# Optimization experiments

Measured on AMD Instinct MI355X. Metric: run time of the kernel, lower is better.

The kernel has to match this reference:

```python
import jax, jax.numpy as jnp
import numpy as np

N = 200000      # nodes
E = 200000      # edges per direction
IN = 256        # in_dim
HID = 256       # hidden_dim
HEADS = 4
C = HID // HEADS  # 64 per-head channels
OUT = 128
EPS = 1e-5      # LayerNorm eps (torch default)


def _ln(x, g, b):
    m = jnp.mean(x, axis=-1, keepdims=True)
    v = jnp.mean(jnp.square(x - m), axis=-1, keepdims=True)
    return (x - m) / jnp.sqrt(v + EPS) * g + b


def _gat(x, W, att_src, att_dst, bias, edge_index):
    """PyG GATConv (default args: add_self_loops=True, negative_slope=0.2, concat heads)."""
    n = x.shape[0]
    loops = jnp.arange(n, dtype=edge_index.dtype)
    ei = jnp.concatenate([edge_index, jnp.stack([loops, loops])], axis=1)
    src, dst = ei[0], ei[1]
    h = (x @ W).reshape(n, HEADS, C)                      # [N,H,C]
    a_src = jnp.sum(h * att_src, axis=-1)                 # [N,H]
    a_dst = jnp.sum(h * att_dst, axis=-1)                 # [N,H]
    e = jax.nn.leaky_relu(a_src[src] + a_dst[dst], 0.2)   # [E+N,H]
    m = jax.ops.segment_max(e, dst, num_segments=n)       # per-dst softmax max
    ex = jnp.exp(e - m[dst])
    denom = jax.ops.segment_sum(ex, dst, num_segments=n)
    alpha = ex / denom[dst]                               # [E+N,H]
    out = jax.ops.segment_sum(h[src] * alpha[..., None], dst, num_segments=n)
    return out.reshape(n, HEADS * C) + bias


def setup_inputs() -> dict:
    key = jax.random.key(0)
    ks = jax.random.split(key, 20)
    w = lambda k, s, sc=0.05: jax.random.normal(k, s, jnp.float32) * sc
    return {
        "x": jax.random.normal(ks[0], (N, IN), jnp.float32),
        "edge_index_bu": jax.random.randint(ks[1], (2, E), 0, N, jnp.int32),
        "edge_index_td": jax.random.randint(ks[2], (2, E), 0, N, jnp.int32),
        "Wp": w(ks[3], (IN, HID)), "bp": jnp.zeros((HID,), jnp.float32),
        "W_bu": w(ks[4], (HID, HID)), "asrc_bu": w(ks[5], (HEADS, C)),
        "adst_bu": w(ks[6], (HEADS, C)), "bias_bu": jnp.zeros((HID,), jnp.float32),
        "W_td": w(ks[7], (HID, HID)), "asrc_td": w(ks[8], (HEADS, C)),
        "adst_td": w(ks[9], (HEADS, C)), "bias_td": jnp.zeros((HID,), jnp.float32),
        "Wf": w(ks[10], (2 * HID, OUT)), "bf": jnp.zeros((OUT,), jnp.float32),
        "g_bu": jnp.ones((HID,), jnp.float32), "b_bu": jnp.zeros((HID,), jnp.float32),
        "g_td": jnp.ones((HID,), jnp.float32), "b_td": jnp.zeros((HID,), jnp.float32),
        "g_out": jnp.ones((OUT,), jnp.float32), "b_out": jnp.zeros((OUT,), jnp.float32),
    }


def reference(x, edge_index_bu, edge_index_td, Wp, bp,
              W_bu, asrc_bu, adst_bu, bias_bu,
              W_td, asrc_td, adst_td, bias_td,
              Wf, bf, g_bu, b_bu, g_td, b_td, g_out, b_out):
    h = jax.nn.relu(x @ Wp + bp)  # dropout is identity in eval
    x_bu = jax.nn.relu(_ln(_gat(h, W_bu, asrc_bu, adst_bu, bias_bu, edge_index_bu), g_bu, b_bu))
    x_td = jax.nn.relu(_ln(_gat(h, W_td, asrc_td, adst_td, bias_td, edge_index_td), g_td, b_td))
    out = jnp.concatenate([x_bu, x_td], axis=-1) @ Wf + bf
    out = _ln(out, g_out, b_out)
    nrm = jnp.sqrt(jnp.sum(jnp.square(out), axis=-1, keepdims=True))
    return out / jnp.maximum(nrm, 1e-12)
```

## Files before the change

### kernel.cpp

```cpp
#include <hip/hip_runtime.h>
#include <hip/hip_bf16.h>
#include <stdint.h>


typedef __attribute__((ext_vector_type(8))) short bf16x8;
typedef __attribute__((ext_vector_type(4))) short bf16x4;
typedef __attribute__((ext_vector_type(4))) float f32x4;

#define HID 256
#define HEADS 4
#define CH 64

__device__ __forceinline__ float wred(float v) {
    #pragma unroll
    for (int o = 32; o > 0; o >>= 1) v += __shfl_xor(v, o, 64);
    return v;
}
__device__ __forceinline__ float red16(float v) {
    #pragma unroll
    for (int o = 1; o < 16; o <<= 1) v += __shfl_xor(v, o, 64);
    return v;
}
__device__ __forceinline__ float bf2f(short s) {
    return __uint_as_float(((unsigned)(unsigned short)s) << 16);
}
__device__ __forceinline__ float sel4(float a0, float a1, float a2, float a3, int h) {
    return h == 0 ? a0 : (h == 1 ? a1 : (h == 2 ? a2 : a3));
}

__device__ __forceinline__ void gload_lds16(const void* g, void* l) {
    __builtin_amdgcn_global_load_lds(
        reinterpret_cast<const __attribute__((address_space(1))) uint32_t*>(
            reinterpret_cast<uintptr_t>(g)),
        reinterpret_cast<__attribute__((address_space(3))) uint32_t*>(
            reinterpret_cast<uintptr_t>(l)),
        16, 0, 0);
}

__global__ __launch_bounds__(256) void cvt_bf16(const float* __restrict__ src,
                                                __hip_bfloat16* __restrict__ dst, long n8) {
    long i = (long)blockIdx.x * 256 + threadIdx.x;
    if (i >= n8) return;
    f32x4 v0 = *(const f32x4*)(src + i * 8);
    f32x4 v1 = *(const f32x4*)(src + i * 8 + 4);
    __hip_bfloat16 o[8];
    o[0] = __float2bfloat16(v0[0]); o[1] = __float2bfloat16(v0[1]);
    o[2] = __float2bfloat16(v0[2]); o[3] = __float2bfloat16(v0[3]);
    o[4] = __float2bfloat16(v1[0]); o[5] = __float2bfloat16(v1[1]);
    o[6] = __float2bfloat16(v1[2]); o[7] = __float2bfloat16(v1[3]);
    *(bf16x8*)((short*)dst + i * 8) = *(const bf16x8*)o;
}

__global__ void transpose_w(const float* __restrict__ W,
                            __hip_bfloat16* __restrict__ Wt, int KI, int KO) {
    int idx = blockIdx.x * 256 + threadIdx.x;
    if (idx >= KI * KO) return;
    int k = idx / KO, j = idx % KO;
    Wt[(long)j * KI + k] = __float2bfloat16(W[idx]);
}

template<int BN, int MODE>
__global__ __launch_bounds__(512) void gemm_tiled(
    const __hip_bfloat16* __restrict__ A0, const __hip_bfloat16* __restrict__ A1,
    int lda, int kSplit,
    const __hip_bfloat16* __restrict__ Bt, int KI,
    const float* __restrict__ bias, int doRelu,
    __hip_bfloat16* __restrict__ outB, float* __restrict__ outF,
    const float* __restrict__ asrcW, const float* __restrict__ adstW,
    float* __restrict__ aS, float* __restrict__ aD,
    const float* __restrict__ gw, const float* __restrict__ bw, int N) {

    constexpr int WN = BN / 64;
    constexpr int WM = 8 / WN;
    constexpr int MR = (128 / WM) / 16;

    __shared__ __align__(16) __hip_bfloat16 sA[128 * 32];
    __shared__ __align__(16) __hip_bfloat16 sB[BN * 32];
    __shared__ float sRed[MODE == 2 ? 128 * 4 : 4];
    __shared__ float sN2[MODE == 2 ? 128 * 2 : 2];

    int tid = threadIdx.x;
    int wv = tid >> 6, ln = tid & 63;
    int m = ln & 15, q = ln >> 4;
    long row0 = (long)blockIdx.x * 128;
    int wr = (wv / WN) * (128 / WM);
    int wc = (wv % WN) * 64;

    f32x4 acc[MR][4];
    #pragma unroll
    for (int mi = 0; mi < MR; ++mi)
        #pragma unroll
        for (int t = 0; t < 4; ++t) acc[mi][t] = (f32x4){0.f, 0.f, 0.f, 0.f};

    int oA = tid * 16;
    long rowA = row0 + (oA >> 6);
    if (rowA >= N) rowA = N - 1;
    long aOff = rowA * lda + ((oA & 63) >> 1);

    for (int k0 = 0; k0 < KI; k0 += 32) {
        const __hip_bfloat16* Ab = (k0 < kSplit) ? A0 + k0 : A1 + (k0 - kSplit);
        __syncthreads();
        gload_lds16(Ab + aOff, (char*)sA + oA);
        #pragma unroll
        for (int j = 0; j < BN / 128; ++j) {
            int o = j * 8192 + tid * 16;
            const __hip_bfloat16* src = Bt + (long)(o >> 6) * KI + k0 + ((o & 63) >> 1);
            gload_lds16(src, (char*)sB + o);
        }
        __syncthreads();

        bf16x8 af[MR], bfr[4];
        #pragma unroll
        for (int mi = 0; mi < MR; ++mi)
            af[mi] = *(const bf16x8*)((const char*)sA + ((wr + mi * 16 + m) << 6) + q * 16);
        #pragma unroll
        for (int t = 0; t < 4; ++t)
            bfr[t] = *(const bf16x8*)((const char*)sB + ((wc + t * 16 + m) << 6) + q * 16);
        #pragma unroll
        for (int mi = 0; mi < MR; ++mi)
            #pragma unroll
            for (int t = 0; t < 4; ++t)
                acc[mi][t] = __builtin_amdgcn_mfma_f32_16x16x32_bf16(af[mi], bfr[t],
                                                                     acc[mi][t], 0, 0, 0);
    }

    if constexpr (MODE != 2) {
        #pragma unroll
        for (int mi = 0; mi < MR; ++mi) {
            #pragma unroll
            for (int t = 0; t < 4; ++t) {
                int col = wc + t * 16 + m;
                float bv = bias ? bias[col] : 0.f;
                #pragma unroll
                for (int r = 0; r < 4; ++r) {
                    long row = row0 + wr + mi * 16 + q * 4 + r;
                    if (row < N) {
                        float v = acc[mi][t][r] + bv;
                        if (doRelu) v = fmaxf(v, 0.f);
                        outB[row * BN + col] = __float2bfloat16(v);
                    }
                }
            }
        }
    }

    if constexpr (MODE == 1) {
        int h = wc >> 6;
        f32x4 sw, dw;
        #pragma unroll
        for (int t = 0; t < 4; ++t) {
            sw[t] = asrcW[wc + t * 16 + m];
            dw[t] = adstW[wc + t * 16 + m];
        }
        #pragma unroll
        for (int mi = 0; mi < MR; ++mi) {
            #pragma unroll
            for (int r = 0; r < 4; ++r) {
                float ps = acc[mi][0][r] * sw[0] + acc[mi][1][r] * sw[1]
                         + acc[mi][2][r] * sw[2] + acc[mi][3][r] * sw[3];
                float pd = acc[mi][0][r] * dw[0] + acc[mi][1][r] * dw[1]
                         + acc[mi][2][r] * dw[2] + acc[mi][3][r] * dw[3];
                ps = red16(ps); pd = red16(pd);
                long row = row0 + wr + mi * 16 + q * 4 + r;
                if (m == 0 && row < N) {
                    aS[row * 4 + h] = ps;
                    aD[row * 4 + h] = pd;
                }
            }
        }
    }

    if constexpr (MODE == 2) {
        float vv[MR][4][4];
        float gcol[4], bcol[4];
        #pragma unroll
        for (int t = 0; t < 4; ++t) {
            int col = wc + t * 16 + m;
            float bb = bias[col];
            gcol[t] = gw[col]; bcol[t] = bw[col];
            #pragma unroll
            for (int mi = 0; mi < MR; ++mi)
                #pragma unroll
                for (int r = 0; r < 4; ++r) vv[mi][t][r] = acc[mi][t][r] + bb;
        }
        int wcid = wc >> 6;
        #pragma unroll
        for (int mi = 0; mi < MR; ++mi) {
            #pragma unroll
            for (int r = 0; r < 4; ++r) {
                float s1 = vv[mi][0][r] + vv[mi][1][r] + vv[mi][2][r] + vv[mi][3][r];
                float s2 = vv[mi][0][r] * vv[mi][0][r] + vv[mi][1][r] * vv[mi][1][r]
                         + vv[mi][2][r] * vv[mi][2][r] + vv[mi][3][r] * vv[mi][3][r];
                s1 = red16(s1); s2 = red16(s2);
                if (m == 0) {
                    int lrow = wr + mi * 16 + q * 4 + r;
                    sRed[lrow * 4 + wcid * 2 + 0] = s1;
                    sRed[lrow * 4 + wcid * 2 + 1] = s2;
                }
            }
        }
        __syncthreads();
        #pragma unroll
        for (int mi = 0; mi < MR; ++mi) {
            #pragma unroll
            for (int r = 0; r < 4; ++r) {
                int lrow = wr + mi * 16 + q * 4 + r;
                float S1 = sRed[lrow * 4 + 0] + sRed[lrow * 4 + 2];
                float S2 = sRed[lrow * 4 + 1] + sRed[lrow * 4 + 3];
                float mean = S1 * (1.f / 128.f);
                float var = S2 * (1.f / 128.f) - mean * mean;
                float inv = rsqrtf(fmaxf(var, 0.f) + 1e-5f);
                float n2 = 0.f;
                #pragma unroll
                for (int t = 0; t < 4; ++t) {
                    float y = (vv[mi][t][r] - mean) * inv * gcol[t] + bcol[t];
                    vv[mi][t][r] = y;
                    n2 += y * y;
                }
                n2 = red16(n2);
                if (m == 0) sN2[lrow * 2 + wcid] = n2;
            }
        }
        __syncthreads();
        #pragma unroll
        for (int mi = 0; mi < MR; ++mi) {
            #pragma unroll
            for (int r = 0; r < 4; ++r) {
                int lrow = wr + mi * 16 + q * 4 + r;
                long row = row0 + lrow;
                float nrm = sqrtf(sN2[lrow * 2] + sN2[lrow * 2 + 1]);
                float sc = 1.f / fmaxf(nrm, 1e-12f);
                if (row < N) {
                    #pragma unroll
                    for (int t = 0; t < 4; ++t)
                        outF[row * 128 + wc + t * 16 + m] = vv[mi][t][r] * sc;
                }
            }
        }
    }
}

__global__ __launch_bounds__(256) void hist_dst(const int* __restrict__ ei, int E,
                                                int* __restrict__ cnt) {
    int e = blockIdx.x * 256 + threadIdx.x;
    if (e < E) atomicAdd(&cnt[ei[E + e]], 1);
}

__global__ __launch_bounds__(256) void scan1(const int* __restrict__ cnt,
                                             int* __restrict__ offpart,
                                             int* __restrict__ bsum, int n) {
    int t = threadIdx.x, i = blockIdx.x * 256 + t;
    int lane = t & 63, w = t >> 6;
    int v = (i < n) ? cnt[i] : 0;
    int inc = v;
    #pragma unroll
    for (int o = 1; o < 64; o <<= 1) {
        int u = __shfl_up(inc, o, 64);
        if (lane >= o) inc += u;
    }
    __shared__ int wsum[4];
    if (lane == 63) wsum[w] = inc;
    __syncthreads();
    int wadd = 0;
    #pragma unroll
    for (int k = 0; k < 4; ++k) if (k < w) wadd += wsum[k];
    if (i < n) offpart[i] = inc - v + wadd;
    if (t == 255) bsum[blockIdx.x] = inc + wadd;
}

__global__ __launch_bounds__(256) void scan2(const int* __restrict__ bsum,
                                             int* __restrict__ btot, int nb) {
    int t = threadIdx.x, lane = t & 63, w = t >> 6;
    int loc[4]; int s = 0;
    #pragma unroll
    for (int k = 0; k < 4; ++k) {
        int idx = t * 4 + k;
        int v = (idx < nb) ? bsum[idx] : 0;
        loc[k] = s; s += v;
    }
    int inc = s;
    #pragma unroll
    for (int o = 1; o < 64; o <<= 1) {
        int u = __shfl_up(inc, o, 64);
        if (lane >= o) inc += u;
    }
    __shared__ int wsum[4];
    if (lane == 63) wsum[w] = inc;
    __syncthreads();
    int wadd = 0;
    #pragma unroll
    for (int k = 0; k < 4; ++k) if (k < w) wadd += wsum[k];
    int excl = inc - s + wadd;
    #pragma unroll
    for (int k = 0; k < 4; ++k) {
        int idx = t * 4 + k;
        if (idx < nb) btot[idx] = excl + loc[k];
    }
}

__global__ __launch_bounds__(256) void finalize_off(const int* __restrict__ offpart,
                                                    const int* __restrict__ btot,
                                                    int* __restrict__ off, int n, int E) {
    int i = blockIdx.x * 256 + threadIdx.x;
    if (i < n) off[i] = offpart[i] + btot[i >> 8];
    if (i == 0) off[n] = E;
}

__global__ __launch_bounds__(256) void scatter_src(const int* __restrict__ ei, int E,
                                                   const int* __restrict__ off,
                                                   int* __restrict__ cur,
                                                   int* __restrict__ esrc) {
    int e = blockIdx.x * 256 + threadIdx.x;
    if (e >= E) return;
    int d = ei[E + e];
    int pos = off[d] + atomicAdd(&cur[d], 1);
    esrc[pos] = ei[e];
}

__global__ __launch_bounds__(256) void gat_gather(
    const int* __restrict__ off, const int* __restrict__ esrc,
    const float* __restrict__ a_s, const float* __restrict__ a_d,
    const __hip_bfloat16* __restrict__ hw,
    const float* __restrict__ bias, const float* __restrict__ g,
    const float* __restrict__ b,
    __hip_bfloat16* __restrict__ out, int N) {
    int lane = threadIdx.x & 63;
    long d = (long)blockIdx.x * 4 + (threadIdx.x >> 6);
    if (d >= N) return;
    int beg = off[d], end = off[d + 1];
    f32x4 adv = *(const f32x4*)(a_d + 4 * d);
    f32x4 asd = *(const f32x4*)(a_s + 4 * d);
    int hh = lane & 3;
    float adh_l = sel4(adv[0], adv[1], adv[2], adv[3], hh);
    float ash_l = sel4(asd[0], asd[1], asd[2], asd[3], hh);
    float es_l = ash_l + adh_l; es_l = es_l > 0.f ? es_l : 0.2f * es_l;
    float m_l = es_l, sum_l = 1.f;
    if (lane < 4) {
        for (int j = beg; j < end; ++j) {
            int s = esrc[j];
            float e = a_s[4 * (long)s + lane] + adh_l;
            e = e > 0.f ? e : 0.2f * e;
            m_l = fmaxf(m_l, e);
        }
        sum_l = __expf(es_l - m_l);
        for (int j = beg; j < end; ++j) {
            int s = esrc[j];
            float e = a_s[4 * (long)s + lane] + adh_l;
            e = e > 0.f ? e : 0.2f * e;
            sum_l += __expf(e - m_l);
        }
    }
    int h4 = lane >> 4;
    float mh = __shfl(m_l, h4, 64);
    float rsh = 1.f / __shfl(sum_l, h4, 64);
    float adh = sel4(adv[0], adv[1], adv[2], adv[3], h4);
    float esh = sel4(asd[0], asd[1], asd[2], asd[3], h4) + adh;
    esh = esh > 0.f ? esh : 0.2f * esh;
    int c0 = lane * 4;
    float acc0, acc1, acc2, acc3;
    {
        float alpha = __expf(esh - mh) * rsh;
        bf16x4 hv = *(const bf16x4*)(hw + d * HID + c0);
        acc0 = alpha * bf2f(hv[0]); acc1 = alpha * bf2f(hv[1]);
        acc2 = alpha * bf2f(hv[2]); acc3 = alpha * bf2f(hv[3]);
    }
    for (int j = beg; j < end; ++j) {
        int s = esrc[j];
        float as_h = a_s[4 * (long)s + h4];
        float e = as_h + adh; e = e > 0.f ? e : 0.2f * e;
        float alpha = __expf(e - mh) * rsh;
        bf16x4 hv = *(const bf16x4*)(hw + (long)s * HID + c0);
        acc0 += alpha * bf2f(hv[0]); acc1 += alpha * bf2f(hv[1]);
        acc2 += alpha * bf2f(hv[2]); acc3 += alpha * bf2f(hv[3]);
    }
    f32x4 bi = *(const f32x4*)(bias + c0);
    acc0 += bi[0]; acc1 += bi[1]; acc2 += bi[2]; acc3 += bi[3];
    float mean = wred(acc0 + acc1 + acc2 + acc3) * (1.f / 256.f);
    acc0 -= mean; acc1 -= mean; acc2 -= mean; acc3 -= mean;
    float var = wred(acc0 * acc0 + acc1 * acc1 + acc2 * acc2 + acc3 * acc3) * (1.f / 256.f);
    float inv = rsqrtf(var + 1e-5f);
    f32x4 gv = *(const f32x4*)(g + c0);
    f32x4 bv = *(const f32x4*)(b + c0);
    __hip_bfloat16 t0 = __float2bfloat16(fmaxf(acc0 * inv * gv[0] + bv[0], 0.f));
    __hip_bfloat16 t1 = __float2bfloat16(fmaxf(acc1 * inv * gv[1] + bv[1], 0.f));
    __hip_bfloat16 t2 = __float2bfloat16(fmaxf(acc2 * inv * gv[2] + bv[2], 0.f));
    __hip_bfloat16 t3 = __float2bfloat16(fmaxf(acc3 * inv * gv[3] + bv[3], 0.f));
    __hip_bfloat16* orow = out + d * HID + c0;
    orow[0] = t0; orow[1] = t1; orow[2] = t2; orow[3] = t3;
}

extern "C" void kernel_launch(void* const* d_in, const int* in_sizes, int n_in,
                              void* d_out, int out_size, void* d_ws, size_t ws_size,
                              hipStream_t stream) {
    const float* x      = (const float*)d_in[0];
    const int*   ei_bu  = (const int*)d_in[1];
    const int*   ei_td  = (const int*)d_in[2];
    const float* Wp     = (const float*)d_in[3];
    const float* bp     = (const float*)d_in[4];
    const float* W_bu   = (const float*)d_in[5];
    const float* asrc_bu= (const float*)d_in[6];
    const float* adst_bu= (const float*)d_in[7];
    const float* bias_bu= (const float*)d_in[8];
    const float* W_td   = (const float*)d_in[9];
    const float* asrc_td= (const float*)d_in[10];
    const float* adst_td= (const float*)d_in[11];
    const float* bias_td= (const float*)d_in[12];
    const float* Wf     = (const float*)d_in[13];
    const float* bfv    = (const float*)d_in[14];
    const float* g_bu   = (const float*)d_in[15];
    const float* b_bu   = (const float*)d_in[16];
    const float* g_td   = (const float*)d_in[17];
    const float* b_td   = (const float*)d_in[18];
    const float* g_out  = (const float*)d_in[19];
    const float* b_out  = (const float*)d_in[20];

    const int N = in_sizes[0] / HID;
    const int E = in_sizes[1] / 2;

    char* ws = (char*)d_ws;
    size_t off0 = 0;
    auto take = [&](size_t bytes) -> char* {
        char* p = ws + off0;
        off0 += (bytes + 255) & ~(size_t)255;
        return p;
    };
    __hip_bfloat16* xbf   = (__hip_bfloat16*)take((size_t)N * HID * 2);
    __hip_bfloat16* h_buf = (__hip_bfloat16*)take((size_t)N * HID * 2);
    __hip_bfloat16* xbu   = (__hip_bfloat16*)take((size_t)N * HID * 2);
    __hip_bfloat16* xtd   = (__hip_bfloat16*)take((size_t)N * HID * 2);
    float* a_s   = (float*)take((size_t)N * 16);
    float* a_d   = (float*)take((size_t)N * 16);
    int* cnt     = (int*)take((size_t)N * 4);
    int* cur     = (int*)take((size_t)N * 4);
    int* offpart = (int*)take((size_t)N * 4);
    int* offarr  = (int*)take((size_t)(N + 1) * 4);
    int* esrc    = (int*)take((size_t)E * 4);
    int* bsum    = (int*)take(1024 * 4);
    int* btot    = (int*)take(1024 * 4);
    __hip_bfloat16* Wpt  = (__hip_bfloat16*)take(256 * 256 * 2);
    __hip_bfloat16* Wbut = (__hip_bfloat16*)take(256 * 256 * 2);
    __hip_bfloat16* Wtdt = (__hip_bfloat16*)take(256 * 256 * 2);
    __hip_bfloat16* Wft  = (__hip_bfloat16*)take(512 * 128 * 2);
    __hip_bfloat16* hw = xbf;

    transpose_w<<<(256 * 256 + 255) / 256, 256, 0, stream>>>(Wp, Wpt, 256, 256);
    transpose_w<<<(256 * 256 + 255) / 256, 256, 0, stream>>>(W_bu, Wbut, 256, 256);
    transpose_w<<<(256 * 256 + 255) / 256, 256, 0, stream>>>(W_td, Wtdt, 256, 256);
    transpose_w<<<(512 * 128 + 255) / 256, 256, 0, stream>>>(Wf, Wft, 512, 128);
    long nx8 = (long)N * HID / 8;
    cvt_bf16<<<(nx8 + 255) / 256, 256, 0, stream>>>(x, xbf, nx8);

    int gm = (N + 127) / 128;

    gemm_tiled<256, 0><<<gm, 512, 0, stream>>>(xbf, xbf, HID, HID, Wpt, HID,
                                               bp, 1, h_buf, nullptr,
                                               nullptr, nullptr, nullptr, nullptr,
                                               nullptr, nullptr, N);

    const int* eis[2] = {ei_bu, ei_td};
    const __hip_bfloat16* Wts[2] = {Wbut, Wtdt};
    const float* asrcs[2] = {asrc_bu, asrc_td};
    const float* adsts[2] = {adst_bu, adst_td};
    const float* biases[2]= {bias_bu, bias_td};
    const float* gs[2]    = {g_bu, g_td};
    const float* bs[2]    = {b_bu, b_td};
    __hip_bfloat16* xouts[2] = {xbu, xtd};

    int egrid = (E + 255) / 256;
    int ngrid = (N + 255) / 256;
    int nb = (N + 255) / 256;
    for (int dir = 0; dir < 2; ++dir) {
        gemm_tiled<256, 1><<<gm, 512, 0, stream>>>(h_buf, h_buf, HID, HID, Wts[dir], HID,
                                                   nullptr, 0, hw, nullptr,
                                                   asrcs[dir], adsts[dir], a_s, a_d,
                                                   nullptr, nullptr, N);
        hipMemsetAsync(cnt, 0, (size_t)N * 8, stream);
        hist_dst<<<egrid, 256, 0, stream>>>(eis[dir], E, cnt);
        scan1<<<nb, 256, 0, stream>>>(cnt, offpart, bsum, N);
        scan2<<<1, 256, 0, stream>>>(bsum, btot, nb);
        finalize_off<<<ngrid, 256, 0, stream>>>(offpart, btot, offarr, N, E);
        scatter_src<<<egrid, 256, 0, stream>>>(eis[dir], E, offarr, cur, esrc);
        gat_gather<<<(N + 3) / 4, 256, 0, stream>>>(offarr, esrc, a_s, a_d, hw,
                                                    biases[dir], gs[dir], bs[dir],
                                                    xouts[dir], N);
    }

    gemm_tiled<128, 2><<<gm, 512, 0, stream>>>(xbu, xtd, HID, HID, Wft, 512,
                                               bfv, 0, nullptr, (float*)d_out,
                                               nullptr, nullptr, nullptr, nullptr,
                                               g_out, b_out, N);
}
```

Measured before the change: 996.8 us.

## Fuse fp32-to-bf16 conversion into GEMM, merge direction GEMMs, precompute attention alphas

Converts x from fp32 to bf16 inside the first GEMM's A-tile load, which removes the separate conversion pass and its bf16 copy. The two GAT projection GEMMs become one 512-wide GEMM with concatenated weights, and it writes attention logits for both directions. A new per-node kernel precomputes the softmax alphas per edge, so the gather kernel only streams features, now with 16 lanes per node and 16 channels each. Outputs go into one concatenated buffer that the final GEMM reads directly. The cost is an extra alpha buffer, a kernel that reads each edge's logits three times, and a one-pass variance formula that is less numerically robust.

```diff
diff --git a/kernel.cpp b/kernel.cpp
--- a/kernel.cpp
+++ b/kernel.cpp
@@ -8,14 +8,7 @@
 typedef __attribute__((ext_vector_type(4))) float f32x4;
 
 #define HID 256
-#define HEADS 4
-#define CH 64
-
-__device__ __forceinline__ float wred(float v) {
-    #pragma unroll
-    for (int o = 32; o > 0; o >>= 1) v += __shfl_xor(v, o, 64);
-    return v;
-}
+
 __device__ __forceinline__ float red16(float v) {
     #pragma unroll
     for (int o = 1; o < 16; o <<= 1) v += __shfl_xor(v, o, 64);
@@ -23,9 +16,6 @@
 }
 __device__ __forceinline__ float bf2f(short s) {
     return __uint_as_float(((unsigned)(unsigned short)s) << 16);
-}
-__device__ __forceinline__ float sel4(float a0, float a1, float a2, float a3, int h) {
-    return h == 0 ? a0 : (h == 1 ? a1 : (h == 2 ? a2 : a3));
 }
 
 __device__ __forceinline__ void gload_lds16(const void* g, void* l) {
@@ -37,20 +27,6 @@
         16, 0, 0);
 }
 
-__global__ __launch_bounds__(256) void cvt_bf16(const float* __restrict__ src,
-                                                __hip_bfloat16* __restrict__ dst, long n8) {
-    long i = (long)blockIdx.x * 256 + threadIdx.x;
-    if (i >= n8) return;
-    f32x4 v0 = *(const f32x4*)(src + i * 8);
-    f32x4 v1 = *(const f32x4*)(src + i * 8 + 4);
-    __hip_bfloat16 o[8];
-    o[0] = __float2bfloat16(v0[0]); o[1] = __float2bfloat16(v0[1]);
-    o[2] = __float2bfloat16(v0[2]); o[3] = __float2bfloat16(v0[3]);
-    o[4] = __float2bfloat16(v1[0]); o[5] = __float2bfloat16(v1[1]);
-    o[6] = __float2bfloat16(v1[2]); o[7] = __float2bfloat16(v1[3]);
-    *(bf16x8*)((short*)dst + i * 8) = *(const bf16x8*)o;
-}
-
 __global__ void transpose_w(const float* __restrict__ W,
                             __hip_bfloat16* __restrict__ Wt, int KI, int KO) {
     int idx = blockIdx.x * 256 + threadIdx.x;
@@ -59,15 +35,16 @@
     Wt[(long)j * KI + k] = __float2bfloat16(W[idx]);
 }
 
-template<int BN, int MODE>
+template<int BN, int MODE, int CVT>
 __global__ __launch_bounds__(512) void gemm_tiled(
-    const __hip_bfloat16* __restrict__ A0, const __hip_bfloat16* __restrict__ A1,
-    int lda, int kSplit,
+    const float* __restrict__ Af, const __hip_bfloat16* __restrict__ Ab, int lda,
     const __hip_bfloat16* __restrict__ Bt, int KI,
     const float* __restrict__ bias, int doRelu,
     __hip_bfloat16* __restrict__ outB, float* __restrict__ outF,
-    const float* __restrict__ asrcW, const float* __restrict__ adstW,
-    float* __restrict__ aS, float* __restrict__ aD,
+    const float* __restrict__ asrc0, const float* __restrict__ adst0,
+    const float* __restrict__ asrc1, const float* __restrict__ adst1,
+    float* __restrict__ aS0, float* __restrict__ aD0,
+    float* __restrict__ aS1, float* __restrict__ aD1,
     const float* __restrict__ gw, const float* __restrict__ bw, int N) {
 
     constexpr int WN = BN / 64;
@@ -95,12 +72,27 @@
     int oA = tid * 16;
     long rowA = row0 + (oA >> 6);
     if (rowA >= N) rowA = N - 1;
-    long aOff = rowA * lda + ((oA & 63) >> 1);
+    int kel = (oA & 63) >> 1;
+    long aBase = rowA * (long)lda + kel;
 
     for (int k0 = 0; k0 < KI; k0 += 32) {
-        const __hip_bfloat16* Ab = (k0 < kSplit) ? A0 + k0 : A1 + (k0 - kSplit);
+        f32x4 fa0, fa1;
+        if constexpr (CVT) {
+            const float* src = Af + aBase + k0;
+            fa0 = *(const f32x4*)src;
+            fa1 = *(const f32x4*)(src + 4);
+        }
         __syncthreads();
-        gload_lds16(Ab + aOff, (char*)sA + oA);
+        if constexpr (CVT) {
+            __hip_bfloat16 t8[8];
+            t8[0] = __float2bfloat16(fa0[0]); t8[1] = __float2bfloat16(fa0[1]);
+            t8[2] = __float2bfloat16(fa0[2]); t8[3] = __float2bfloat16(fa0[3]);
+            t8[4] = __float2bfloat16(fa1[0]); t8[5] = __float2bfloat16(fa1[1]);
+            t8[6] = __float2bfloat16(fa1[2]); t8[7] = __float2bfloat16(fa1[3]);
+            *(bf16x8*)((char*)sA + oA) = *(const bf16x8*)t8;
+        } else {
+            gload_lds16(Ab + aBase + k0, (char*)sA + oA);
+        }
         #pragma unroll
         for (int j = 0; j < BN / 128; ++j) {
             int o = j * 8192 + tid * 16;
@@ -145,12 +137,18 @@
     }
 
     if constexpr (MODE == 1) {
-        int h = wc >> 6;
+        int dir = wc >> 8;
+        int cc = wc & 255;
+        int h = cc >> 6;
+        const float* as_ = dir ? asrc1 : asrc0;
+        const float* ad_ = dir ? adst1 : adst0;
+        float* aS = dir ? aS1 : aS0;
+        float* aD = dir ? aD1 : aD0;
         f32x4 sw, dw;
         #pragma unroll
         for (int t = 0; t < 4; ++t) {
-            sw[t] = asrcW[wc + t * 16 + m];
-            dw[t] = adstW[wc + t * 16 + m];
+            sw[t] = as_[cc + t * 16 + m];
+            dw[t] = ad_[cc + t * 16 + m];
         }
         #pragma unroll
         for (int mi = 0; mi < MR; ++mi) {
@@ -317,76 +315,134 @@
     esrc[pos] = ei[e];
 }
 
+__global__ __launch_bounds__(256) void att_alpha(
+    const int* __restrict__ off, const int* __restrict__ esrc,
+    const float* __restrict__ a_s, const float* __restrict__ a_d,
+    float* __restrict__ alpha_self, float* __restrict__ alpha_e, int N) {
+    int d = blockIdx.x * 256 + threadIdx.x;
+    if (d >= N) return;
+    int beg = off[d], end = off[d + 1];
+    f32x4 adv = *(const f32x4*)(a_d + 4 * (long)d);
+    f32x4 asd = *(const f32x4*)(a_s + 4 * (long)d);
+    float es[4], m[4];
+    #pragma unroll
+    for (int h = 0; h < 4; ++h) {
+        float e = asd[h] + adv[h]; e = e > 0.f ? e : 0.2f * e;
+        es[h] = e; m[h] = e;
+    }
+    for (int j = beg; j < end; ++j) {
+        int s = esrc[j];
+        f32x4 asv = *(const f32x4*)(a_s + 4 * (long)s);
+        #pragma unroll
+        for (int h = 0; h < 4; ++h) {
+            float e = asv[h] + adv[h]; e = e > 0.f ? e : 0.2f * e;
+            m[h] = fmaxf(m[h], e);
+        }
+    }
+    float sum[4];
+    #pragma unroll
+    for (int h = 0; h < 4; ++h) sum[h] = __expf(es[h] - m[h]);
+    for (int j = beg; j < end; ++j) {
+        int s = esrc[j];
+        f32x4 asv = *(const f32x4*)(a_s + 4 * (long)s);
+        #pragma unroll
+        for (int h = 0; h < 4; ++h) {
+            float e = asv[h] + adv[h]; e = e > 0.f ? e : 0.2f * e;
+            sum[h] += __expf(e - m[h]);
+        }
+    }
+    float rs[4];
+    #pragma unroll
+    for (int h = 0; h < 4; ++h) rs[h] = 1.f / sum[h];
+    f32x4 sa;
+    #pragma unroll
+    for (int h = 0; h < 4; ++h) sa[h] = __expf(es[h] - m[h]) * rs[h];
+    *(f32x4*)(alpha_self + 4 * (long)d) = sa;
+    for (int j = beg; j < end; ++j) {
+        int s = esrc[j];
+        f32x4 asv = *(const f32x4*)(a_s + 4 * (long)s);
+        f32x4 av;
+        #pragma unroll
+        for (int h = 0; h < 4; ++h) {
+            float e = asv[h] + adv[h]; e = e > 0.f ? e : 0.2f * e;
+            av[h] = __expf(e - m[h]) * rs[h];
+        }
+        *(f32x4*)(alpha_e + 4 * (long)j) = av;
+    }
+}
+
 __global__ __launch_bounds__(256) void gat_gather(
     const int* __restrict__ off, const int* __restrict__ esrc,
-    const float* __restrict__ a_s, const float* __restrict__ a_d,
-    const __hip_bfloat16* __restrict__ hw,
+    const float* __restrict__ alpha_self, const float* __restrict__ alpha_e,
+    const __hip_bfloat16* __restrict__ hw, int dirOff,
     const float* __restrict__ bias, const float* __restrict__ g,
     const float* __restrict__ b,
     __hip_bfloat16* __restrict__ out, int N) {
-    int lane = threadIdx.x & 63;
-    long d = (long)blockIdx.x * 4 + (threadIdx.x >> 6);
+    int tid = threadIdx.x;
+    int lane = tid & 63;
+    int grp = lane >> 4, li = lane & 15;
+    long d = (long)blockIdx.x * 16 + (tid >> 6) * 4 + grp;
     if (d >= N) return;
     int beg = off[d], end = off[d + 1];
-    f32x4 adv = *(const f32x4*)(a_d + 4 * d);
-    f32x4 asd = *(const f32x4*)(a_s + 4 * d);
-    int hh = lane & 3;
-    float adh_l = sel4(adv[0], adv[1], adv[2], adv[3], hh);
-    float ash_l = sel4(asd[0], asd[1], asd[2], asd[3], hh);
-    float es_l = ash_l + adh_l; es_l = es_l > 0.f ? es_l : 0.2f * es_l;
-    float m_l = es_l, sum_l = 1.f;
-    if (lane < 4) {
-        for (int j = beg; j < end; ++j) {
-            int s = esrc[j];
-            float e = a_s[4 * (long)s + lane] + adh_l;
-            e = e > 0.f ? e : 0.2f * e;
-            m_l = fmaxf(m_l, e);
-        }
-        sum_l = __expf(es_l - m_l);
-        for (int j = beg; j < end; ++j) {
-            int s = esrc[j];
-            float e = a_s[4 * (long)s + lane] + adh_l;
-            e = e > 0.f ? e : 0.2f * e;
-            sum_l += __expf(e - m_l);
-        }
-    }
-    int h4 = lane >> 4;
-    float mh = __shfl(m_l, h4, 64);
-    float rsh = 1.f / __shfl(sum_l, h4, 64);
-    float adh = sel4(adv[0], adv[1], adv[2], adv[3], h4);
-    float esh = sel4(asd[0], asd[1], asd[2], asd[3], h4) + adh;
-    esh = esh > 0.f ? esh : 0.2f * esh;
-    int c0 = lane * 4;
-    float acc0, acc1, acc2, acc3;
+    int head = li >> 2;
+    int c0 = li * 16;
+    float acc[16];
     {
-        float alpha = __expf(esh - mh) * rsh;
-        bf16x4 hv = *(const bf16x4*)(hw + d * HID + c0);
-        acc0 = alpha * bf2f(hv[0]); acc1 = alpha * bf2f(hv[1]);
-        acc2 = alpha * bf2f(hv[2]); acc3 = alpha * bf2f(hv[3]);
+        float a = alpha_self[4 * d + head];
+        const __hip_bfloat16* r = hw + d * 512 + dirOff + c0;
+        bf16x8 h0 = *(const bf16x8*)r;
+        bf16x8 h1 = *(const bf16x8*)(r + 8);
+        #pragma unroll
+        for (int k = 0; k < 8; ++k) {
+            acc[k] = a * bf2f(h0[k]);
+            acc[8 + k] = a * bf2f(h1[k]);
+        }
     }
     for (int j = beg; j < end; ++j) {
         int s = esrc[j];
-        float as_h = a_s[4 * (long)s + h4];
-        float e = as_h + adh; e = e > 0.f ? e : 0.2f * e;
-        float alpha = __expf(e - mh) * rsh;
-        bf16x4 hv = *(const bf16x4*)(hw + (long)s * HID + c0);
-        acc0 += alpha * bf2f(hv[0]); acc1 += alpha * bf2f(hv[1]);
-        acc2 += alpha * bf2f(hv[2]); acc3 += alpha * bf2f(hv[3]);
-    }
-    f32x4 bi = *(const f32x4*)(bias + c0);
-    acc0 += bi[0]; acc1 += bi[1]; acc2 += bi[2]; acc3 += bi[3];
-    float mean = wred(acc0 + acc1 + acc2 + acc3) * (1.f / 256.f);
-    acc0 -= mean; acc1 -= mean; acc2 -= mean; acc3 -= mean;
-    float var = wred(acc0 * acc0 + acc1 * acc1 + acc2 * acc2 + acc3 * acc3) * (1.f / 256.f);
-    float inv = rsqrtf(var + 1e-5f);
-    f32x4 gv = *(const f32x4*)(g + c0);
-    f32x4 bv = *(const f32x4*)(b + c0);
-    __hip_bfloat16 t0 = __float2bfloat16(fmaxf(acc0 * inv * gv[0] + bv[0], 0.f));
-    __hip_bfloat16 t1 = __float2bfloat16(fmaxf(acc1 * inv * gv[1] + bv[1], 0.f));
-    __hip_bfloat16 t2 = __float2bfloat16(fmaxf(acc2 * inv * gv[2] + bv[2], 0.f));
-    __hip_bfloat16 t3 = __float2bfloat16(fmaxf(acc3 * inv * gv[3] + bv[3], 0.f));
-    __hip_bfloat16* orow = out + d * HID + c0;
-    orow[0] = t0; orow[1] = t1; orow[2] = t2; orow[3] = t3;
+        float a = alpha_e[4 * (long)j + head];
+        const __hip_bfloat16* r = hw + (long)s * 512 + dirOff + c0;
+        bf16x8 h0 = *(const bf16x8*)r;
+        bf16x8 h1 = *(const bf16x8*)(r + 8);
+        #pragma unroll
+        for (int k = 0; k < 8; ++k) {
+            acc[k] += a * bf2f(h0[k]);
+            acc[8 + k] += a * bf2f(h1[k]);
+        }
+    }
+    float s1 = 0.f, s2 = 0.f;
+    #pragma unroll
+    for (int k = 0; k < 16; k += 4) {
+        f32x4 bi = *(const f32x4*)(bias + c0 + k);
+        #pragma unroll
+        for (int u = 0; u < 4; ++u) {
+            float v = acc[k + u] + bi[u];
+            acc[k + u] = v;
+            s1 += v; s2 += v * v;
+        }
+    }
+    #pragma unroll
+    for (int o = 1; o < 16; o <<= 1) {
+        s1 += __shfl_xor(s1, o, 64);
+        s2 += __shfl_xor(s2, o, 64);
+    }
+    float mean = s1 * (1.f / 256.f);
+    float var = s2 * (1.f / 256.f) - mean * mean;
+    float inv = rsqrtf(fmaxf(var, 0.f) + 1e-5f);
+    __hip_bfloat16 o16[16];
+    #pragma unroll
+    for (int k = 0; k < 16; k += 4) {
+        f32x4 gv = *(const f32x4*)(g + c0 + k);
+        f32x4 bv = *(const f32x4*)(b + c0 + k);
+        #pragma unroll
+        for (int u = 0; u < 4; ++u) {
+            float y = (acc[k + u] - mean) * inv * gv[u] + bv[u];
+            o16[k + u] = __float2bfloat16(fmaxf(y, 0.f));
+        }
+    }
+    __hip_bfloat16* orow = out + d * 512 + dirOff + c0;
+    *(bf16x8*)orow = *(const bf16x8*)o16;
+    *(bf16x8*)(orow + 8) = *(const bf16x8*)(o16 + 8);
 }
 
 extern "C" void kernel_launch(void* const* d_in, const int* in_sizes, int n_in,
@@ -424,12 +480,15 @@
         off0 += (bytes + 255) & ~(size_t)255;
         return p;
     };
-    __hip_bfloat16* xbf   = (__hip_bfloat16*)take((size_t)N * HID * 2);
-    __hip_bfloat16* h_buf = (__hip_bfloat16*)take((size_t)N * HID * 2);
-    __hip_bfloat16* xbu   = (__hip_bfloat16*)take((size_t)N * HID * 2);
-    __hip_bfloat16* xtd   = (__hip_bfloat16*)take((size_t)N * HID * 2);
-    float* a_s   = (float*)take((size_t)N * 16);
-    float* a_d   = (float*)take((size_t)N * 16);
+    __hip_bfloat16* h_buf = (__hip_bfloat16*)take((size_t)N * 256 * 2);
+    __hip_bfloat16* hwcat = (__hip_bfloat16*)take((size_t)N * 512 * 2);
+    __hip_bfloat16* xcat  = (__hip_bfloat16*)take((size_t)N * 512 * 2);
+    float* aS0   = (float*)take((size_t)N * 16);
+    float* aD0   = (float*)take((size_t)N * 16);
+    float* aS1   = (float*)take((size_t)N * 16);
+    float* aD1   = (float*)take((size_t)N * 16);
+    float* alsf  = (float*)take((size_t)N * 16);
+    float* ale   = (float*)take((size_t)E * 16);
     int* cnt     = (int*)take((size_t)N * 4);
     int* cur     = (int*)take((size_t)N * 4);
     int* offpart = (int*)take((size_t)N * 4);
@@ -438,55 +497,53 @@
     int* bsum    = (int*)take(1024 * 4);
     int* btot    = (int*)take(1024 * 4);
     __hip_bfloat16* Wpt  = (__hip_bfloat16*)take(256 * 256 * 2);
-    __hip_bfloat16* Wbut = (__hip_bfloat16*)take(256 * 256 * 2);
-    __hip_bfloat16* Wtdt = (__hip_bfloat16*)take(256 * 256 * 2);
-    __hip_bfloat16* Wft  = (__hip_bfloat16*)take(512 * 128 * 2);
-    __hip_bfloat16* hw = xbf;
+    __hip_bfloat16* Wcat = (__hip_bfloat16*)take(512 * 256 * 2);
+    __hip_bfloat16* Wft  = (__hip_bfloat16*)take(128 * 512 * 2);
 
     transpose_w<<<(256 * 256 + 255) / 256, 256, 0, stream>>>(Wp, Wpt, 256, 256);
-    transpose_w<<<(256 * 256 + 255) / 256, 256, 0, stream>>>(W_bu, Wbut, 256, 256);
-    transpose_w<<<(256 * 256 + 255) / 256, 256, 0, stream>>>(W_td, Wtdt, 256, 256);
+    transpose_w<<<(256 * 256 + 255) / 256, 256, 0, stream>>>(W_bu, Wcat, 256, 256);
+    transpose_w<<<(256 * 256 + 255) / 256, 256, 0, stream>>>(W_td, Wcat + 256 * 256, 256, 256);
     transpose_w<<<(512 * 128 + 255) / 256, 256, 0, stream>>>(Wf, Wft, 512, 128);
-    long nx8 = (long)N * HID / 8;
-    cvt_bf16<<<(nx8 + 255) / 256, 256, 0, stream>>>(x, xbf, nx8);
 
     int gm = (N + 127) / 128;
 
-    gemm_tiled<256, 0><<<gm, 512, 0, stream>>>(xbf, xbf, HID, HID, Wpt, HID,
-                                               bp, 1, h_buf, nullptr,
-                                               nullptr, nullptr, nullptr, nullptr,
-                                               nullptr, nullptr, N);
+    gemm_tiled<256, 0, 1><<<gm, 512, 0, stream>>>(
+        x, nullptr, 256, Wpt, 256, bp, 1, h_buf, nullptr,
+        nullptr, nullptr, nullptr, nullptr, nullptr, nullptr, nullptr, nullptr,
+        nullptr, nullptr, N);
+
+    gemm_tiled<512, 1, 0><<<gm, 512, 0, stream>>>(
+        nullptr, h_buf, 256, Wcat, 256, nullptr, 0, hwcat, nullptr,
+        asrc_bu, adst_bu, asrc_td, adst_td, aS0, aD0, aS1, aD1,
+        nullptr, nullptr, N);
 
     const int* eis[2] = {ei_bu, ei_td};
-    const __hip_bfloat16* Wts[2] = {Wbut, Wtdt};
-    const float* asrcs[2] = {asrc_bu, asrc_td};
-    const float* adsts[2] = {adst_bu, adst_td};
+    const float* aSs[2] = {aS0, aS1};
+    const float* aDs[2] = {aD0, aD1};
     const float* biases[2]= {bias_bu, bias_td};
     const float* gs[2]    = {g_bu, g_td};
     const float* bs[2]    = {b_bu, b_td};
-    __hip_bfloat16* xouts[2] = {xbu, xtd};
 
     int egrid = (E + 255) / 256;
     int ngrid = (N + 255) / 256;
     int nb = (N + 255) / 256;
     for (int dir = 0; dir < 2; ++dir) {
-        gemm_tiled<256, 1><<<gm, 512, 0, stream>>>(h_buf, h_buf, HID, HID, Wts[dir], HID,
-                                                   nullptr, 0, hw, nullptr,
-                                                   asrcs[dir], adsts[dir], a_s, a_d,
-                                                   nullptr, nullptr, N);
         hipMemsetAsync(cnt, 0, (size_t)N * 8, stream);
         hist_dst<<<egrid, 256, 0, stream>>>(eis[dir], E, cnt);
         scan1<<<nb, 256, 0, stream>>>(cnt, offpart, bsum, N);
         scan2<<<1, 256, 0, stream>>>(bsum, btot, nb);
         finalize_off<<<ngrid, 256, 0, stream>>>(offpart, btot, offarr, N, E);
         scatter_src<<<egrid, 256, 0, stream>>>(eis[dir], E, offarr, cur, esrc);
-        gat_gather<<<(N + 3) / 4, 256, 0, stream>>>(offarr, esrc, a_s, a_d, hw,
-                                                    biases[dir], gs[dir], bs[dir],
-                                                    xouts[dir], N);
-    }
-
-    gemm_tiled<128, 2><<<gm, 512, 0, stream>>>(xbu, xtd, HID, HID, Wft, 512,
-                                               bfv, 0, nullptr, (float*)d_out,
-                                               nullptr, nullptr, nullptr, nullptr,
-                                               g_out, b_out, N);
-}
+        att_alpha<<<ngrid, 256, 0, stream>>>(offarr, esrc, aSs[dir], aDs[dir],
+                                             alsf, ale, N);
+        gat_gather<<<(N + 15) / 16, 256, 0, stream>>>(offarr, esrc, alsf, ale,
+                                                      hwcat, dir * 256,
+                                                      biases[dir], gs[dir], bs[dir],
+                                                      xcat, N);
+    }
+
+    gemm_tiled<128, 2, 0><<<gm, 512, 0, stream>>>(
+        nullptr, xcat, 512, Wft, 512, bfv, 0, nullptr, (float*)d_out,
+        nullptr, nullptr, nullptr, nullptr, nullptr, nullptr, nullptr, nullptr,
+        g_out, b_out, N);
+}
```

Result: faster. 955.2 us (-4.2%).
